# Kernel optimization log

Hardware: AMD Instinct MI355X
Metric: run time of the kernel (lower is better)

Reference implementation:

```python
import jax, jax.numpy as jnp
import numpy as np

KERNEL_SIZE = 5  # k, local correlation window
EPS = 1e-6


def local_self_correlation(x, k):
    """x: (b,c,h,w) -> (b,k^2,h,w). For each of the k^2 shifts (dy,dx) compute
    sum_c x[..., y+dy, x+dx] * x[..., y, x] with zero padding at borders."""
    pad = k // 2
    b, c, h, w = x.shape
    xp = jnp.pad(x, ((0, 0), (0, 0), (pad, pad), (pad, pad)))
    outs = []
    for dy in range(-pad, pad + 1):  # fixed small loop over k^2 shifts
        for dx in range(-pad, pad + 1):
            nb = xp[:, :, pad + dy:pad + dy + h, pad + dx:pad + dx + w]
            outs.append(jnp.sum(nb * x, axis=1))  # (b,h,w)
    return jnp.stack(outs, axis=1)  # (b,k^2,h,w)


def feature_l2norm(f):
    norm = jnp.sqrt(jnp.sum(f * f, axis=1, keepdims=True) + EPS)
    return f / norm


def setup_inputs() -> dict:
    key = jax.random.key(0)
    k1, k2, k3 = jax.random.split(key, 3)
    b, c, h, w = 8, 1024, 64, 64
    hidden = 1024
    in_dim = c + KERNEL_SIZE * KERNEL_SIZE  # 1049
    x = jax.random.normal(k1, (b, c, h, w), dtype=jnp.float32)
    W = jax.random.normal(k2, (hidden, in_dim), dtype=jnp.float32) * 0.02
    bias = jax.random.normal(k3, (hidden,), dtype=jnp.float32) * 0.02
    return {"x": x, "W": W, "b": bias}


def reference(x, W, b):
    feature_gs = local_self_correlation(x, KERNEL_SIZE)      # (b,k^2,h,w)
    feature_gs = feature_l2norm(feature_gs)
    feature_cat = jnp.concatenate([x, feature_gs], axis=1)    # (b,c+k^2,h,w)
    # 1x1 conv == channel GEMM, then ReLU
    out = jnp.einsum('bihw,oi->bohw', feature_cat, W) + b[None, :, None, None]
    return jax.nn.relu(out)
```

## Files before the change

### kernel.cpp

```cpp
#include <hip/hip_runtime.h>

typedef __attribute__((ext_vector_type(8))) short bf16x8;
typedef __attribute__((ext_vector_type(4))) float f32x4;

__device__ __forceinline__ unsigned short f2bf(float f) {
    unsigned int u = __float_as_uint(f);
    unsigned int r = (u + 0x7fffu + ((u >> 16) & 1u)) >> 16;
    return (unsigned short)r;
}

#define KPAD 1088
#define NT   17

__global__ void kWb_conv(const float* __restrict__ W, unsigned short* __restrict__ Wb)
{
    const int o = blockIdx.x;
    for (int k = threadIdx.x; k < KPAD; k += 256) {
        float v = (k < 1049) ? W[(size_t)o * 1049 + k] : 0.f;
        Wb[(size_t)o * KPAD + k] = f2bf(v);
    }
}

__global__ __launch_bounds__(256) void kT_conv(const float* __restrict__ x,
                                               unsigned short* __restrict__ xT)
{
    __shared__ unsigned short tile[64][128];
    const int bid = blockIdx.x;
    const int mst = bid >> 3;
    const int ct  = bid & 7;
    const int m0  = mst * 64;
    const int b   = m0 >> 12, ms0 = m0 & 4095;
    const int t   = threadIdx.x;
    const int msq = (t & 15) * 4;
    const int cg  = t >> 4;
    const int c0  = ct * 128 + cg * 8;

    const float* src = x + ((size_t)b * 1024 + c0) * 4096 + ms0 + msq;
    float4 v[8];
    #pragma unroll
    for (int j = 0; j < 8; ++j)
        v[j] = *(const float4*)(src + (size_t)j * 4096);

    #pragma unroll
    for (int p = 0; p < 4; ++p) {
        unsigned int w[4];
        #pragma unroll
        for (int q = 0; q < 4; ++q) {
            float lo = ((const float*)&v[2 * q])[p];
            float hi = ((const float*)&v[2 * q + 1])[p];
            w[q] = (unsigned int)f2bf(lo) | ((unsigned int)f2bf(hi) << 16);
        }
        const int row = msq + p;
        const int pch = cg ^ ((row >> 2) & 15);
        *(uint4*)&tile[row][pch * 8] = make_uint4(w[0], w[1], w[2], w[3]);
    }
    __syncthreads();

    #pragma unroll
    for (int q = 0; q < 4; ++q) {
        const int flat = q * 256 + t;
        const int row  = flat >> 4, ch = flat & 15;
        const int pch  = ch ^ ((row >> 2) & 15);
        uint4 val = *(const uint4*)&tile[row][pch * 8];
        *(uint4*)((char*)xT + (size_t)(m0 + row) * (KPAD * 2) + (size_t)(ct * 128 + ch * 8) * 2) = val;
    }
}

__global__ __launch_bounds__(256, 2) void k1a_corr(const float* __restrict__ x,
                                                   float* __restrict__ fpart)
{
    __shared__ float slab[2][20][68];
    const int bid   = blockIdx.x;
    const int split = bid & 15;
    const int b     = (bid >> 4) & 7;
    const int rg    = bid >> 7;
    const int y0    = rg * 16;
    const int t     = threadIdx.x;
    const int tc    = t & 15, tr = t >> 4;
    const int cs    = tc * 4;

    if (t < 160) {
        int buf = t / 80, rem = t % 80;
        int r = rem >> 2, cc = rem & 3;
        slab[buf][r][(cc < 2) ? cc : (64 + cc)] = 0.f;
    }

    float acc[25][4];
    #pragma unroll
    for (int s = 0; s < 25; ++s)
        #pragma unroll
        for (int p = 0; p < 4; ++p) acc[s][p] = 0.f;

    const float* xb = x + ((size_t)b * 1024 + split * 64) * 4096;

    auto stage = [&](int i, int buf) {
        const float* src = xb + (size_t)i * 4096;
        #pragma unroll
        for (int pass = 0; pass < 2; ++pass) {
            int idx = t + pass * 256;
            if (idx < 320) {
                int r = idx >> 4, c4 = idx & 15;
                int y = y0 - 2 + r;
                float4 v = make_float4(0.f, 0.f, 0.f, 0.f);
                if (y >= 0 && y < 64) v = *(const float4*)(src + y * 64 + c4 * 4);
                float2* dst = (float2*)&slab[buf][r][2 + c4 * 4];
                dst[0] = make_float2(v.x, v.y);
                dst[1] = make_float2(v.z, v.w);
            }
        }
    };

    stage(0, 0);
    for (int i = 0; i < 64; ++i) {
        __syncthreads();
        if (i + 1 < 64) stage(i + 1, (i + 1) & 1);
        const int buf = i & 1;
        const float* base = &slab[buf][tr][cs];

        float ctr[4], wf[8];
        {
            const float4* pr = (const float4*)(base + 2 * 68);
            float4 a = pr[0], b4 = pr[1];
            wf[0]=a.x; wf[1]=a.y; wf[2]=a.z; wf[3]=a.w;
            wf[4]=b4.x; wf[5]=b4.y; wf[6]=b4.z; wf[7]=b4.w;
            ctr[0]=wf[2]; ctr[1]=wf[3]; ctr[2]=wf[4]; ctr[3]=wf[5];
            #pragma unroll
            for (int dx = -2; dx <= 2; ++dx)
                #pragma unroll
                for (int p = 0; p < 4; ++p)
                    acc[10 + dx + 2][p] += wf[p + 2 + dx] * ctr[p];
        }
        #pragma unroll
        for (int r = 0; r < 5; ++r) {
            if (r == 2) continue;
            const float4* pr = (const float4*)(base + r * 68);
            float4 a = pr[0], b4 = pr[1];
            wf[0]=a.x; wf[1]=a.y; wf[2]=a.z; wf[3]=a.w;
            wf[4]=b4.x; wf[5]=b4.y; wf[6]=b4.z; wf[7]=b4.w;
            #pragma unroll
            for (int dx = -2; dx <= 2; ++dx)
                #pragma unroll
                for (int p = 0; p < 4; ++p)
                    acc[r * 5 + dx + 2][p] += wf[p + 2 + dx] * ctr[p];
        }
    }

    const int mbase = b * 4096 + (y0 + tr) * 64 + cs;
    #pragma unroll
    for (int s = 0; s < 25; ++s) {
        *(float4*)(fpart + (size_t)(split * 25 + s) * 32768 + mbase) =
            make_float4(acc[s][0], acc[s][1], acc[s][2], acc[s][3]);
    }
}

__global__ void k1b_norm(const float* __restrict__ fpart, unsigned short* __restrict__ xT)
{
    const int m = blockIdx.x * 256 + threadIdx.x;
    float f[25];
    #pragma unroll
    for (int s = 0; s < 25; ++s) {
        float v = 0.f;
        #pragma unroll
        for (int sp = 0; sp < 16; ++sp)
            v += fpart[(size_t)(sp * 25 + s) * 32768 + m];
        f[s] = v;
    }
    float ss = 1e-6f;
    #pragma unroll
    for (int s = 0; s < 25; ++s) ss += f[s] * f[s];
    const float inv = 1.f / sqrtf(ss);

    unsigned int w[16];
    #pragma unroll
    for (int q = 0; q < 16; ++q) w[q] = 0u;
    #pragma unroll
    for (int s = 0; s < 25; ++s) {
        unsigned int h = f2bf(f[s] * inv);
        w[s >> 1] |= h << ((s & 1) * 16);
    }
    uint4* dst = (uint4*)((char*)xT + (size_t)m * (KPAD * 2) + 2048);
    dst[0] = make_uint4(w[0],  w[1],  w[2],  w[3]);
    dst[1] = make_uint4(w[4],  w[5],  w[6],  w[7]);
    dst[2] = make_uint4(w[8],  w[9],  w[10], w[11]);
    dst[3] = make_uint4(w[12], w[13], w[14], w[15]);
    uint4 z = make_uint4(0u, 0u, 0u, 0u);
    dst[4] = z; dst[5] = z; dst[6] = z; dst[7] = z;
}

__global__ __launch_bounds__(512, 2) void kgemm(const unsigned short* __restrict__ xT,
                                                const unsigned short* __restrict__ Wb,
                                                const float* __restrict__ bias,
                                                float* __restrict__ out)
{
    __shared__ unsigned short LA[2][256][64];
    __shared__ unsigned short LB[2][256][64];

    const int bid = blockIdx.x;
    const int wg  = (bid & 7) * 64 + (bid >> 3);
    const int mt  = wg >> 2, nt = wg & 3;
    const int m0  = mt * 256, n0 = nt * 256;
    const int t   = threadIdx.x;
    const int l   = t & 63, w = t >> 6;
    const int lr  = l & 15, kq = l >> 4;
    const int wm  = w >> 2, wn = w & 3;

    const int sr = l >> 3;
    const int sp = (l & 7) ^ sr;
    const unsigned short* gA = xT + (size_t)(m0 + w * 8 + sr) * KPAD + sp * 8;
    const unsigned short* gB = Wb + (size_t)(n0 + w * 8 + sr) * KPAD + sp * 8;

    auto STAGE = [&](int tt, int half) {
        if ((unsigned)tt >= NT) return;
        const int db = tt & 1;
        const size_t ko = (size_t)tt * 64;
        if (half < 2) {
            const unsigned short* g = gA + (size_t)(half * 128) * KPAD + ko;
            __builtin_amdgcn_global_load_lds((const void*)g,
                (void*)&LA[db][half * 128 + w * 8][0], 16, 0, 0);
            __builtin_amdgcn_global_load_lds((const void*)(g + (size_t)64 * KPAD),
                (void*)&LA[db][half * 128 + 64 + w * 8][0], 16, 0, 0);
        } else {
            const int hb = half - 2;
            const unsigned short* g = gB + (size_t)(hb * 128) * KPAD + ko;
            __builtin_amdgcn_global_load_lds((const void*)g,
                (void*)&LB[db][hb * 128 + w * 8][0], 16, 0, 0);
            __builtin_amdgcn_global_load_lds((const void*)(g + (size_t)64 * KPAD),
                (void*)&LB[db][hb * 128 + 64 + w * 8][0], 16, 0, 0);
        }
    };

    f32x4 zero = {0.f, 0.f, 0.f, 0.f};
    f32x4 acc[8][4];
    #pragma unroll
    for (int i = 0; i < 8; ++i)
        #pragma unroll
        for (int j = 0; j < 4; ++j) acc[i][j] = zero;

    bf16x8 a0[4][2], a1[4][2], b0[2][2], b1[2][2];

    #define LDA(dst, db, ih)                                                     \
        _Pragma("unroll")                                                        \
        for (int i = 0; i < 4; ++i) {                                            \
            _Pragma("unroll")                                                    \
            for (int ks = 0; ks < 2; ++ks) {                                     \
                const int row = wm * 128 + ((ih) * 4 + i) * 16 + lr;             \
                const int slot = (ks * 4 + kq) ^ (row & 7);                      \
                dst[i][ks] = *(const bf16x8*)&LA[db][row][slot * 8];             \
            }                                                                    \
        }
    #define LDB(dst, db, jh)                                                     \
        _Pragma("unroll")                                                        \
        for (int j = 0; j < 2; ++j) {                                            \
            _Pragma("unroll")                                                    \
            for (int ks = 0; ks < 2; ++ks) {                                     \
                const int row = wn * 64 + ((jh) * 2 + j) * 16 + lr;              \
                const int slot = (ks * 4 + kq) ^ (row & 7);                      \
                dst[j][ks] = *(const bf16x8*)&LB[db][row][slot * 8];             \
            }                                                                    \
        }
    #define MM(A, B, i0, j0)                                                     \
        _Pragma("unroll")                                                        \
        for (int ks = 0; ks < 2; ++ks) {                                         \
            _Pragma("unroll")                                                    \
            for (int i = 0; i < 4; ++i) {                                        \
                _Pragma("unroll")                                                \
                for (int j = 0; j < 2; ++j)                                      \
                    acc[(i0) + i][(j0) + j] = __builtin_amdgcn_mfma_f32_16x16x32_bf16( \
                        A[i][ks], B[j][ks], acc[(i0) + i][(j0) + j], 0, 0, 0);   \
            }                                                                    \
        }
    #define PH_OPEN()                                                            \
        asm volatile("s_barrier" ::: "memory");                                  \
        asm volatile("s_waitcnt lgkmcnt(0)" ::: "memory");                       \
        __builtin_amdgcn_sched_barrier(0);                                       \
        __builtin_amdgcn_s_setprio(1);
    #define PH_CLOSE()                                                           \
        __builtin_amdgcn_s_setprio(0);                                           \
        asm volatile("s_barrier" ::: "memory");

    STAGE(0, 0); STAGE(0, 1); STAGE(0, 2); STAGE(0, 3);
    STAGE(1, 2); STAGE(1, 3);
    asm volatile("s_waitcnt vmcnt(4)" ::: "memory");
    asm volatile("s_barrier" ::: "memory");

    for (int tt = 0; tt < NT; ++tt) {
        const int db = tt & 1;
        LDA(a0, db, 0)
        LDB(b0, db, 0)
        STAGE(tt + 1, 0);
        PH_OPEN()
        MM(a0, b0, 0, 0)
        PH_CLOSE()
        LDB(b1, db, 1)
        STAGE(tt + 1, 1);
        PH_OPEN()
        MM(a0, b1, 0, 2)
        PH_CLOSE()
        LDA(a1, db, 1)
        STAGE(tt + 2, 2);
        PH_OPEN()
        MM(a1, b1, 4, 2)
        PH_CLOSE()
        STAGE(tt + 2, 3);
        asm volatile("s_barrier" ::: "memory");
        asm volatile("s_waitcnt lgkmcnt(0)" ::: "memory");
        __builtin_amdgcn_sched_barrier(0);
        __builtin_amdgcn_s_setprio(1);
        MM(a1, b0, 4, 0)
        __builtin_amdgcn_s_setprio(0);
        if (tt + 2 < NT) {
            asm volatile("s_waitcnt vmcnt(4)" ::: "memory");
        } else {
            asm volatile("s_waitcnt vmcnt(0)" ::: "memory");
        }
        asm volatile("s_barrier" ::: "memory");
    }

    const int bb = m0 >> 12;
    const int ms = (m0 & 4095) + wm * 128 + kq * 4;
    #pragma unroll
    for (int j = 0; j < 4; ++j) {
        const int n = n0 + wn * 64 + j * 16 + lr;
        const float bv = bias[n];
        float* ob = out + (size_t)bb * 4194304 + (size_t)n * 4096 + ms;
        #pragma unroll
        for (int i = 0; i < 8; ++i) {
            f32x4 v = acc[i][j];
            float4 o = make_float4(fmaxf(v[0] + bv, 0.f), fmaxf(v[1] + bv, 0.f),
                                   fmaxf(v[2] + bv, 0.f), fmaxf(v[3] + bv, 0.f));
            *(float4*)(ob + i * 16) = o;
        }
    }
    #undef LDA
    #undef LDB
    #undef MM
    #undef PH_OPEN
    #undef PH_CLOSE
}

extern "C" void kernel_launch(void* const* d_in, const int* in_sizes, int n_in,
                              void* d_out, int out_size, void* d_ws, size_t ws_size,
                              hipStream_t stream)
{
    const float* x    = (const float*)d_in[0];
    const float* W    = (const float*)d_in[1];
    const float* bias = (const float*)d_in[2];
    float* out        = (float*)d_out;

    char* ws = (char*)d_ws;
    unsigned short* xT = (unsigned short*)ws;
    unsigned short* Wb = (unsigned short*)(ws + 71303168);
    float* fpart       = (float*)d_out;

    kWb_conv<<<1024, 256, 0, stream>>>(W, Wb);
    kT_conv <<<4096, 256, 0, stream>>>(x, xT);
    k1a_corr<<<512,  256, 0, stream>>>(x, fpart);
    k1b_norm<<<128,  256, 0, stream>>>(fpart, xT);
    kgemm   <<<512,  512, 0, stream>>>(xT, Wb, bias, out);
}
```

Baseline: 234.8 us.

## Register-prefetch correlation slabs and software-pipeline LDS fragment loads in GEMM

The correlation kernel now loads the next channels' global data into registers two steps ahead and writes them to shared memory before computing, so global load latency overlaps the FMA work. The GEMM main loop is reordered so that the A/B fragment LDS reads for the next K-tile are issued under the current tile's MFMAs. Partial lgkmcnt waits replace the full waits. This hides LDS and global latency at the cost of more live registers and tricky barrier/waitcnt correctness.

```diff
diff --git a/kernel.cpp b/kernel.cpp
--- a/kernel.cpp
+++ b/kernel.cpp
@@ -93,57 +93,83 @@
 
     const float* xb = x + ((size_t)b * 1024 + split * 64) * 4096;
 
-    auto stage = [&](int i, int buf) {
-        const float* src = xb + (size_t)i * 4096;
-        #pragma unroll
-        for (int pass = 0; pass < 2; ++pass) {
-            int idx = t + pass * 256;
-            if (idx < 320) {
-                int r = idx >> 4, c4 = idx & 15;
-                int y = y0 - 2 + r;
-                float4 v = make_float4(0.f, 0.f, 0.f, 0.f);
-                if (y >= 0 && y < 64) v = *(const float4*)(src + y * 64 + c4 * 4);
-                float2* dst = (float2*)&slab[buf][r][2 + c4 * 4];
-                dst[0] = make_float2(v.x, v.y);
-                dst[1] = make_float2(v.z, v.w);
-            }
-        }
-    };
-
-    stage(0, 0);
-    for (int i = 0; i < 64; ++i) {
+    const int r0 = t >> 4,         c40 = t & 15;
+    const int y0r0 = y0 - 2 + r0;
+    const int r1 = (t + 256) >> 4, c41 = t & 15;
+    const int y0r1 = y0 - 2 + r1;
+    const bool has1 = (t < 64);
+
+    #define K1A_LOAD(ch, VA, VB)                                                \
+        {                                                                        \
+            const float* s_ = xb + (size_t)(ch) * 4096;                          \
+            VA = (y0r0 >= 0 && y0r0 < 64) ? *(const float4*)(s_ + y0r0 * 64 + c40 * 4) \
+                                          : make_float4(0.f, 0.f, 0.f, 0.f);     \
+            if (has1)                                                            \
+                VB = (y0r1 >= 0 && y0r1 < 64) ? *(const float4*)(s_ + y0r1 * 64 + c41 * 4) \
+                                              : make_float4(0.f, 0.f, 0.f, 0.f); \
+        }
+    #define K1A_WRITE(buf, VA, VB)                                               \
+        {                                                                        \
+            float2* d0 = (float2*)&slab[buf][r0][2 + c40 * 4];                   \
+            d0[0] = make_float2(VA.x, VA.y);                                     \
+            d0[1] = make_float2(VA.z, VA.w);                                     \
+            if (has1) {                                                          \
+                float2* d1 = (float2*)&slab[buf][r1][2 + c41 * 4];               \
+                d1[0] = make_float2(VB.x, VB.y);                                 \
+                d1[1] = make_float2(VB.z, VB.w);                                 \
+            }                                                                    \
+        }
+    #define K1A_COMPUTE(buf)                                                     \
+        {                                                                        \
+            const float* base = &slab[buf][tr][cs];                              \
+            float ctr[4], wf[8];                                                 \
+            {                                                                    \
+                const float4* pr = (const float4*)(base + 2 * 68);               \
+                float4 a = pr[0], b4 = pr[1];                                    \
+                wf[0]=a.x; wf[1]=a.y; wf[2]=a.z; wf[3]=a.w;                      \
+                wf[4]=b4.x; wf[5]=b4.y; wf[6]=b4.z; wf[7]=b4.w;                  \
+                ctr[0]=wf[2]; ctr[1]=wf[3]; ctr[2]=wf[4]; ctr[3]=wf[5];          \
+                _Pragma("unroll")                                                \
+                for (int dx = -2; dx <= 2; ++dx)                                 \
+                    _Pragma("unroll")                                            \
+                    for (int p = 0; p < 4; ++p)                                  \
+                        acc[10 + dx + 2][p] += wf[p + 2 + dx] * ctr[p];          \
+            }                                                                    \
+            _Pragma("unroll")                                                    \
+            for (int r = 0; r < 5; ++r) {                                        \
+                if (r == 2) continue;                                            \
+                const float4* pr = (const float4*)(base + r * 68);               \
+                float4 a = pr[0], b4 = pr[1];                                    \
+                wf[0]=a.x; wf[1]=a.y; wf[2]=a.z; wf[3]=a.w;                      \
+                wf[4]=b4.x; wf[5]=b4.y; wf[6]=b4.z; wf[7]=b4.w;                  \
+                _Pragma("unroll")                                                \
+                for (int dx = -2; dx <= 2; ++dx)                                 \
+                    _Pragma("unroll")                                            \
+                    for (int p = 0; p < 4; ++p)                                  \
+                        acc[r * 5 + dx + 2][p] += wf[p + 2 + dx] * ctr[p];       \
+            }                                                                    \
+        }
+
+    float4 Sa0, Sa1, Sb0, Sb1;
+    K1A_LOAD(0, Sa0, Sa1)
+    K1A_LOAD(1, Sb0, Sb1)
+    K1A_WRITE(0, Sa0, Sa1)
+    K1A_LOAD(2, Sa0, Sa1)
+    __syncthreads();
+
+    for (int i = 0; i < 64; i += 2) {
+        K1A_WRITE(1, Sb0, Sb1)
+        K1A_LOAD(min(i + 3, 63), Sb0, Sb1)
+        K1A_COMPUTE(0)
         __syncthreads();
-        if (i + 1 < 64) stage(i + 1, (i + 1) & 1);
-        const int buf = i & 1;
-        const float* base = &slab[buf][tr][cs];
-
-        float ctr[4], wf[8];
-        {
-            const float4* pr = (const float4*)(base + 2 * 68);
-            float4 a = pr[0], b4 = pr[1];
-            wf[0]=a.x; wf[1]=a.y; wf[2]=a.z; wf[3]=a.w;
-            wf[4]=b4.x; wf[5]=b4.y; wf[6]=b4.z; wf[7]=b4.w;
-            ctr[0]=wf[2]; ctr[1]=wf[3]; ctr[2]=wf[4]; ctr[3]=wf[5];
-            #pragma unroll
-            for (int dx = -2; dx <= 2; ++dx)
-                #pragma unroll
-                for (int p = 0; p < 4; ++p)
-                    acc[10 + dx + 2][p] += wf[p + 2 + dx] * ctr[p];
-        }
-        #pragma unroll
-        for (int r = 0; r < 5; ++r) {
-            if (r == 2) continue;
-            const float4* pr = (const float4*)(base + r * 68);
-            float4 a = pr[0], b4 = pr[1];
-            wf[0]=a.x; wf[1]=a.y; wf[2]=a.z; wf[3]=a.w;
-            wf[4]=b4.x; wf[5]=b4.y; wf[6]=b4.z; wf[7]=b4.w;
-            #pragma unroll
-            for (int dx = -2; dx <= 2; ++dx)
-                #pragma unroll
-                for (int p = 0; p < 4; ++p)
-                    acc[r * 5 + dx + 2][p] += wf[p + 2 + dx] * ctr[p];
-        }
-    }
+        K1A_WRITE(0, Sa0, Sa1)
+        K1A_LOAD(min(i + 4, 63), Sa0, Sa1)
+        K1A_COMPUTE(1)
+        __syncthreads();
+    }
+    #undef K1A_LOAD
+    #undef K1A_WRITE
+    #undef K1A_COMPUTE
 
     const int mbase = b * 4096 + (y0 + tr) * 64 + cs;
     #pragma unroll
@@ -238,24 +264,24 @@
 
     bf16x8 a0[4][2], a1[4][2], b0[2][2], b1[2][2];
 
-    #define LDA(dst, db, ih)                                                     \
+    #define LDA(dst, dbuf, ih)                                                   \
         _Pragma("unroll")                                                        \
         for (int i = 0; i < 4; ++i) {                                            \
             _Pragma("unroll")                                                    \
             for (int ks = 0; ks < 2; ++ks) {                                     \
                 const int row = wm * 128 + ((ih) * 4 + i) * 16 + lr;             \
                 const int slot = (ks * 4 + kq) ^ (row & 7);                      \
-                dst[i][ks] = *(const bf16x8*)&LA[db][row][slot * 8];             \
-            }                                                                    \
-        }
-    #define LDB(dst, db, jh)                                                     \
+                dst[i][ks] = *(const bf16x8*)&LA[dbuf][row][slot * 8];           \
+            }                                                                    \
+        }
+    #define LDB(dst, dbuf, jh)                                                   \
         _Pragma("unroll")                                                        \
         for (int j = 0; j < 2; ++j) {                                            \
             _Pragma("unroll")                                                    \
             for (int ks = 0; ks < 2; ++ks) {                                     \
                 const int row = wn * 64 + ((jh) * 2 + j) * 16 + lr;              \
                 const int slot = (ks * 4 + kq) ^ (row & 7);                      \
-                dst[j][ks] = *(const bf16x8*)&LB[db][row][slot * 8];             \
+                dst[j][ks] = *(const bf16x8*)&LB[dbuf][row][slot * 8];           \
             }                                                                    \
         }
     #define MM(A, B, i0, j0)                                                     \
@@ -269,51 +295,57 @@
                         A[i][ks], B[j][ks], acc[(i0) + i][(j0) + j], 0, 0, 0);   \
             }                                                                    \
         }
-    #define PH_OPEN()                                                            \
-        asm volatile("s_barrier" ::: "memory");                                  \
-        asm volatile("s_waitcnt lgkmcnt(0)" ::: "memory");                       \
-        __builtin_amdgcn_sched_barrier(0);                                       \
-        __builtin_amdgcn_s_setprio(1);
-    #define PH_CLOSE()                                                           \
-        __builtin_amdgcn_s_setprio(0);                                           \
-        asm volatile("s_barrier" ::: "memory");
+    #define BAR()  asm volatile("s_barrier" ::: "memory");
+    #define LGKM(n) asm volatile("s_waitcnt lgkmcnt(" #n ")" ::: "memory");      \
+                    __builtin_amdgcn_sched_barrier(0);
 
     STAGE(0, 0); STAGE(0, 1); STAGE(0, 2); STAGE(0, 3);
     STAGE(1, 2); STAGE(1, 3);
     asm volatile("s_waitcnt vmcnt(4)" ::: "memory");
-    asm volatile("s_barrier" ::: "memory");
+    BAR()
+    LDA(a0, 0, 0)
+    LDB(b0, 0, 0)
+    LDB(b1, 0, 1)
 
     for (int tt = 0; tt < NT; ++tt) {
         const int db = tt & 1;
-        LDA(a0, db, 0)
-        LDB(b0, db, 0)
         STAGE(tt + 1, 0);
-        PH_OPEN()
+        STAGE(tt + 1, 1);
+        BAR()
+        LGKM(4)
+        __builtin_amdgcn_s_setprio(1);
         MM(a0, b0, 0, 0)
-        PH_CLOSE()
-        LDB(b1, db, 1)
-        STAGE(tt + 1, 1);
-        PH_OPEN()
-        MM(a0, b1, 0, 2)
-        PH_CLOSE()
+        __builtin_amdgcn_s_setprio(0);
+        BAR()
         LDA(a1, db, 1)
         STAGE(tt + 2, 2);
-        PH_OPEN()
-        MM(a1, b1, 4, 2)
-        PH_CLOSE()
+        BAR()
+        LGKM(8)
+        __builtin_amdgcn_s_setprio(1);
+        MM(a0, b1, 0, 2)
+        __builtin_amdgcn_s_setprio(0);
+        BAR()
         STAGE(tt + 2, 3);
-        asm volatile("s_barrier" ::: "memory");
-        asm volatile("s_waitcnt lgkmcnt(0)" ::: "memory");
-        __builtin_amdgcn_sched_barrier(0);
-        __builtin_amdgcn_s_setprio(1);
-        MM(a1, b0, 4, 0)
-        __builtin_amdgcn_s_setprio(0);
         if (tt + 2 < NT) {
             asm volatile("s_waitcnt vmcnt(4)" ::: "memory");
         } else {
             asm volatile("s_waitcnt vmcnt(0)" ::: "memory");
         }
-        asm volatile("s_barrier" ::: "memory");
+        BAR()
+        LGKM(0)
+        __builtin_amdgcn_s_setprio(1);
+        MM(a1, b1, 4, 2)
+        __builtin_amdgcn_sched_barrier(0);
+        if (tt + 1 < NT) { LDA(a0, db ^ 1, 0) }
+        __builtin_amdgcn_s_setprio(0);
+        BAR()
+        LGKM(8)
+        __builtin_amdgcn_s_setprio(1);
+        MM(a1, b0, 4, 0)
+        __builtin_amdgcn_sched_barrier(0);
+        if (tt + 1 < NT) { LDB(b0, db ^ 1, 0) LDB(b1, db ^ 1, 1) }
+        __builtin_amdgcn_s_setprio(0);
+        BAR()
     }
 
     const int bb = m0 >> 12;
@@ -334,8 +366,8 @@
     #undef LDA
     #undef LDB
     #undef MM
-    #undef PH_OPEN
-    #undef PH_CLOSE
+    #undef BAR
+    #undef LGKM
 }
 
 extern "C" void kernel_launch(void* const* d_in, const int* in_sizes, int n_in,
```

Result: faster. 220.6 us (-6.0%).
